# Optimization experiments

Hardware: AMD Instinct MI355X
Metric: run time of the kernel (lower is better)

Reference implementation:

```python
import jax, jax.numpy as jnp
import numpy as np

N_VOXELS = 1024
N_RAYS = 2048
SH_DEGREE = 2
N_SH = 9            # (sh_degree+1)^2 with degree-2 real SH basis (1+3+5 terms)
S = 8               # ray_samples_per_voxel
BG_COLOR = (0.0, 0.0, 0.0)
FAR_PLANE = 100.0
EARLY_STOP_T = 0.01 # transmittance early-termination threshold from the torch loop


def eval_sh_basis(degree, dirs):
    # dirs: [..., 3] -> [..., N_SH]
    x, y, z = dirs[..., 0], dirs[..., 1], dirs[..., 2]
    sh = [jnp.ones_like(x)]
    if degree >= 1:
        sh += [y, z, x]
    if degree >= 2:
        sh += [x * y, y * z, 3 * z ** 2 - 1, x * z, x ** 2 - y ** 2]
    if degree >= 3:
        sh += [y * (3 * x ** 2 - y ** 2), x * y * z, y * (5 * z ** 2 - 1),
               z * (5 * z ** 2 - 3), x * (5 * z ** 2 - 1), (x ** 2 - y ** 2) * z,
               x * (x ** 2 - 3 * y ** 2)]
    return jnp.stack(sh, axis=-1)


def setup_inputs() -> dict:
    key = jax.random.key(0)
    ks = jax.random.split(key, 6)
    positions = jax.random.uniform(ks[0], (N_VOXELS, 3), minval=-1.0, maxval=1.0)
    sizes = 0.05 + 0.15 * jax.random.uniform(ks[1], (N_VOXELS,))
    densities = jax.random.normal(ks[2], (N_VOXELS,))
    colors = 0.3 * jax.random.normal(ks[3], (N_VOXELS, 3 * N_SH))
    ray_origins = jnp.array([0.0, 0.0, -3.0]) + 0.1 * jax.random.normal(ks[4], (N_RAYS, 3))
    targets = jax.random.uniform(ks[5], (N_RAYS, 3), minval=-1.0, maxval=1.0)
    d = targets - ray_origins
    ray_directions = d / jnp.linalg.norm(d, axis=-1, keepdims=True)
    return {"positions": positions, "sizes": sizes, "densities": densities,
            "colors": colors, "ray_origins": ray_origins, "ray_directions": ray_directions}


def _forward(positions, sizes, densities, colors, ray_o, ray_d):
    B = ray_o.shape[0]
    N = positions.shape[0]
    # ---- AABB intersection for all (ray, voxel) pairs ----
    half = (sizes / 2.0)[:, None]                      # [N,1]
    bmin = positions - half                            # [N,3]
    bmax = positions + half
    inv_d = 1.0 / ray_d                                # [B,3]
    t0 = (bmin[None, :, :] - ray_o[:, None, :]) * inv_d[:, None, :]   # [B,N,3]
    t1 = (bmax[None, :, :] - ray_o[:, None, :]) * inv_d[:, None, :]
    t_near = jnp.max(jnp.minimum(t0, t1), axis=-1)     # [B,N]
    t_far = jnp.min(jnp.maximum(t0, t1), axis=-1)
    valid = (t_far > t_near) & (t_far > 0.0)
    # sanitize invalid entries so no inf/nan leaks into masked-out math
    tn = jnp.where(valid, t_near, 0.0)
    tf = jnp.where(valid, t_far, 1.0)

    # ---- per-ray SH color (rgb_samples is constant across samples: dirs = ray_d) ----
    sh = eval_sh_basis(SH_DEGREE, ray_d)               # [B,C]
    coeffs = colors.reshape(N, 3, N_SH)                # [N,3,C]
    rgb_vox = jax.nn.sigmoid(jnp.einsum('bc,nkc->bnk', sh, coeffs))   # [B,N,3]

    # ---- within-voxel alpha compositing (S samples, constant sigma per voxel) ----
    sigma = jnp.exp(densities)                         # [N], density_activation='exp'
    delta = (tf - tn) / S                              # [B,N]
    alpha = 1.0 - jnp.exp(-sigma[None, :] * delta)     # [B,N]
    base = 1.0 - alpha + 1e-8
    i = jnp.arange(S, dtype=jnp.float32)
    pw = base[..., None] ** i                          # [B,N,S] exclusive cumprod of (1-a)
    w = alpha[..., None] * pw                          # per-sample weights
    frac = i / (S - 1)                                 # linspace(t_near, t_far, S)
    t_s = tn[..., None] + (tf - tn)[..., None] * frac  # [B,N,S]
    ws = jnp.where(valid, jnp.sum(w, -1), 0.0)         # [B,N] weight_sum per voxel
    depth_vox = jnp.where(valid, jnp.sum(w * t_s, -1), 0.0)

    # ---- sort voxels per ray by entry distance (invalid -> end) ----
    key_t = jnp.where(valid, tn, jnp.inf)
    order = jnp.argsort(key_t, axis=-1)                # [B,N]
    ws_s = jnp.take_along_axis(ws, order, -1)
    dep_s = jnp.take_along_axis(depth_vox, order, -1)
    rgb_s = jnp.take_along_axis(rgb_vox, order[..., None], 1)

    # ---- sequential compositing across voxels (closed form, with early-stop mask) ----
    one_m = 1.0 - ws_s
    T_before = jnp.cumprod(
        jnp.concatenate([jnp.ones((B, 1), one_m.dtype), one_m[:, :-1]], -1), axis=-1)
    proc = (T_before >= EARLY_STOP_T).astype(one_m.dtype)  # voxels processed before break
    contrib = T_before * ws_s * proc                   # [B,N]
    rgb_acc = jnp.einsum('bn,bnk->bk', contrib, rgb_s) # [B,3]
    depth_acc = jnp.sum(T_before * proc * dep_s, -1)   # [B]
    weight_acc = jnp.sum(contrib, -1)                  # [B]
    T_final = jnp.prod(1.0 - ws_s * proc, -1)          # transmittance at break/end

    bg = jnp.asarray(BG_COLOR, dtype=rgb_acc.dtype)
    rgb_acc = rgb_acc + T_final[:, None] * bg
    has_hit = valid.any(-1)
    depth = jnp.where(has_hit, depth_acc, FAR_PLANE)[:, None]
    return rgb_acc, depth, weight_acc[:, None]


def reference(positions, sizes, densities, colors, ray_origins, ray_directions):
    return _forward(positions, sizes, densities, colors, ray_origins, ray_directions)
```

## Files before the change

### kernel.cpp

```cpp
#include <hip/hip_runtime.h>


#define BLOCK 256
#define CAP   128
#define EARLY_STOP 0.01f

__global__ __launch_bounds__(BLOCK) void voxel_raster(
    const float* __restrict__ positions, const float* __restrict__ sizes,
    const float* __restrict__ densities, const float* __restrict__ colors,
    const float* __restrict__ ray_o, const float* __restrict__ ray_d,
    float* __restrict__ out, int B)
{
    const int b   = blockIdx.x;
    const int tid = threadIdx.x;

    __shared__ int cnt;
    __shared__ unsigned long long key[CAP];
    __shared__ float h_ws[CAP], h_dep[CAP], h_r[CAP], h_g[CAP], h_b[CAP];

    if (tid == 0) cnt = 0;
    __syncthreads();

    const float ox = ray_o[b*3+0], oy = ray_o[b*3+1], oz = ray_o[b*3+2];
    const float dx = ray_d[b*3+0], dy = ray_d[b*3+1], dz = ray_d[b*3+2];
    const float ivx = 1.0f/dx, ivy = 1.0f/dy, ivz = 1.0f/dz;

    float sh[9];
    sh[0]=1.0f; sh[1]=dy; sh[2]=dz; sh[3]=dx;
    sh[4]=dx*dy; sh[5]=dy*dz; sh[6]=3.0f*dz*dz-1.0f; sh[7]=dx*dz; sh[8]=dx*dx-dy*dy;

    const float4 P0 = ((const float4*)positions)[tid*3+0];
    const float4 P1 = ((const float4*)positions)[tid*3+1];
    const float4 P2 = ((const float4*)positions)[tid*3+2];
    const float4 SZ = ((const float4*)sizes)[tid];

    const float pxa[4] = {P0.x, P0.w, P1.z, P2.y};
    const float pya[4] = {P0.y, P1.x, P1.w, P2.z};
    const float pza[4] = {P0.z, P1.y, P2.x, P2.w};
    const float hsa[4] = {SZ.x*0.5f, SZ.y*0.5f, SZ.z*0.5f, SZ.w*0.5f};

    #pragma unroll
    for (int k = 0; k < 4; ++k) {
        const int n = tid*4 + k;
        const float half = hsa[k];
        const float px = pxa[k], py = pya[k], pz = pza[k];

        float a0 = (px - half - ox) * ivx, a1 = (px + half - ox) * ivx;
        float tn = fminf(a0, a1), tf = fmaxf(a0, a1);
        a0 = (py - half - oy) * ivy; a1 = (py + half - oy) * ivy;
        tn = fmaxf(tn, fminf(a0, a1)); tf = fminf(tf, fmaxf(a0, a1));
        a0 = (pz - half - oz) * ivz; a1 = (pz + half - oz) * ivz;
        tn = fmaxf(tn, fminf(a0, a1)); tf = fminf(tf, fmaxf(a0, a1));

        if ((tf > tn) && (tf > 0.0f)) {
            const float sigma = __expf(densities[n]);
            const float dt    = tf - tn;
            const float alpha = 1.0f - __expf(-sigma * dt * 0.125f);
            const float base  = 1.0f - alpha + 1e-8f;
            float pw = 1.0f, ws = 0.0f, dep = 0.0f;
            #pragma unroll
            for (int i = 0; i < 8; i++) {
                const float w  = alpha * pw;
                const float ts = tn + dt * ((float)i * (1.0f / 7.0f));
                ws  += w;
                dep += w * ts;
                pw  *= base;
            }
            float rgb[3];
            #pragma unroll
            for (int c3 = 0; c3 < 3; c3++) {
                float acc = 0.0f;
                #pragma unroll
                for (int c = 0; c < 9; c++)
                    acc += sh[c] * colors[n*27 + c3*9 + c];
                rgb[c3] = __fdividef(1.0f, 1.0f + __expf(-acc));
            }

            const int slot = atomicAdd(&cnt, 1);
            if (slot < CAP) {
                unsigned u = __float_as_uint(tn);
                u = (u & 0x80000000u) ? ~u : (u | 0x80000000u);
                key[slot]   = ((unsigned long long)u << 32) | (unsigned)n;
                h_ws[slot]  = ws;
                h_dep[slot] = dep;
                h_r[slot]   = rgb[0];
                h_g[slot]   = rgb[1];
                h_b[slot]   = rgb[2];
            }
        }
    }
    __syncthreads();

    const int total = cnt;
    const int m = (total < CAP) ? total : CAP;

    if (tid < 64) {
        float ra = 0.f, ga = 0.f, ba = 0.f, da = 0.f, wa = 0.f;
        for (int l = tid; l < m; l += 64) {
            const unsigned long long kl = key[l];
            float Tb = 1.0f;
            for (int j = 0; j < m; ++j) {
                const unsigned long long kj = key[j];
                const float wj = h_ws[j];
                Tb *= (kj < kl) ? (1.0f - wj) : 1.0f;
            }
            if (Tb >= EARLY_STOP) {
                const float ws = h_ws[l];
                const float c  = Tb * ws;
                ra += c * h_r[l];
                ga += c * h_g[l];
                ba += c * h_b[l];
                da += Tb * h_dep[l];
                wa += c;
            }
        }
        #pragma unroll
        for (int off = 32; off > 0; off >>= 1) {
            ra += __shfl_down(ra, off, 64);
            ga += __shfl_down(ga, off, 64);
            ba += __shfl_down(ba, off, 64);
            da += __shfl_down(da, off, 64);
            wa += __shfl_down(wa, off, 64);
        }
        if (tid == 0) {
            out[b*3+0] = ra;
            out[b*3+1] = ga;
            out[b*3+2] = ba;
            out[B*3+b] = (total > 0) ? da : 100.0f;
            out[B*4+b] = wa;
        }
    }
}

extern "C" void kernel_launch(void* const* d_in, const int* in_sizes, int n_in,
                              void* d_out, int out_size, void* d_ws, size_t ws_size,
                              hipStream_t stream) {
    const float* positions = (const float*)d_in[0];
    const float* sizes     = (const float*)d_in[1];
    const float* densities = (const float*)d_in[2];
    const float* colors    = (const float*)d_in[3];
    const float* ray_o     = (const float*)d_in[4];
    const float* ray_d     = (const float*)d_in[5];
    const int B = in_sizes[4] / 3;

    voxel_raster<<<B, BLOCK, 0, stream>>>(
        positions, sizes, densities, colors, ray_o, ray_d, (float*)d_out, B);
}
```

Before: 69.94 us.

## Process four rays per block with one wavefront compositing each ray

Each block now handles four rays. Every thread intersects its four voxels against all four rays, and only the hit lists (tn, tf, key) go into shared memory. Afterwards each wavefront takes one ray and computes density weights and SH colors for that ray's hits, so the color work runs only on hits that pass early stop. Compositing is spread over all four wavefronts instead of leaving three idle, and voxel loads are amortized across rays. In exchange, per-thread register use rises (27 color values, ray arrays) and there are fewer blocks.

```diff
diff --git a/kernel.cpp b/kernel.cpp
--- a/kernel.cpp
+++ b/kernel.cpp
@@ -2,6 +2,7 @@
 
 
 #define BLOCK 256
+#define RPB   4
 #define CAP   128
 #define EARLY_STOP 0.01f
 
@@ -11,23 +12,17 @@
     const float* __restrict__ ray_o, const float* __restrict__ ray_d,
     float* __restrict__ out, int B)
 {
-    const int b   = blockIdx.x;
-    const int tid = threadIdx.x;
-
-    __shared__ int cnt;
-    __shared__ unsigned long long key[CAP];
-    __shared__ float h_ws[CAP], h_dep[CAP], h_r[CAP], h_g[CAP], h_b[CAP];
-
-    if (tid == 0) cnt = 0;
+    const int tid   = threadIdx.x;
+    const int lane  = tid & 63;
+    const int wv    = tid >> 6;
+    const int rbase = blockIdx.x * RPB;
+
+    __shared__ int cnt[RPB];
+    __shared__ unsigned long long key[RPB][CAP];
+    __shared__ float h_tn[RPB][CAP], h_tf[RPB][CAP], h_ws[RPB][CAP];
+
+    if (tid < RPB) cnt[tid] = 0;
     __syncthreads();
-
-    const float ox = ray_o[b*3+0], oy = ray_o[b*3+1], oz = ray_o[b*3+2];
-    const float dx = ray_d[b*3+0], dy = ray_d[b*3+1], dz = ray_d[b*3+2];
-    const float ivx = 1.0f/dx, ivy = 1.0f/dy, ivz = 1.0f/dz;
-
-    float sh[9];
-    sh[0]=1.0f; sh[1]=dy; sh[2]=dz; sh[3]=dx;
-    sh[4]=dx*dy; sh[5]=dy*dz; sh[6]=3.0f*dz*dz-1.0f; sh[7]=dx*dz; sh[8]=dx*dx-dy*dy;
 
     const float4 P0 = ((const float4*)positions)[tid*3+0];
     const float4 P1 = ((const float4*)positions)[tid*3+1];
@@ -39,81 +34,148 @@
     const float pza[4] = {P0.z, P1.y, P2.x, P2.w};
     const float hsa[4] = {SZ.x*0.5f, SZ.y*0.5f, SZ.z*0.5f, SZ.w*0.5f};
 
+    float rox[RPB], roy[RPB], roz[RPB], rix[RPB], riy[RPB], riz[RPB];
+    #pragma unroll
+    for (int r = 0; r < RPB; ++r) {
+        const int b = (rbase + r < B) ? (rbase + r) : 0;
+        rox[r] = ray_o[b*3+0]; roy[r] = ray_o[b*3+1]; roz[r] = ray_o[b*3+2];
+        rix[r] = 1.0f / ray_d[b*3+0];
+        riy[r] = 1.0f / ray_d[b*3+1];
+        riz[r] = 1.0f / ray_d[b*3+2];
+    }
+
     #pragma unroll
     for (int k = 0; k < 4; ++k) {
         const int n = tid*4 + k;
-        const float half = hsa[k];
-        const float px = pxa[k], py = pya[k], pz = pza[k];
-
-        float a0 = (px - half - ox) * ivx, a1 = (px + half - ox) * ivx;
-        float tn = fminf(a0, a1), tf = fmaxf(a0, a1);
-        a0 = (py - half - oy) * ivy; a1 = (py + half - oy) * ivy;
-        tn = fmaxf(tn, fminf(a0, a1)); tf = fminf(tf, fmaxf(a0, a1));
-        a0 = (pz - half - oz) * ivz; a1 = (pz + half - oz) * ivz;
-        tn = fmaxf(tn, fminf(a0, a1)); tf = fminf(tf, fmaxf(a0, a1));
-
-        if ((tf > tn) && (tf > 0.0f)) {
+        const float lox = pxa[k]-hsa[k], hix = pxa[k]+hsa[k];
+        const float loy = pya[k]-hsa[k], hiy = pya[k]+hsa[k];
+        const float loz = pza[k]-hsa[k], hiz = pza[k]+hsa[k];
+        #pragma unroll
+        for (int r = 0; r < RPB; ++r) {
+            float a0 = (lox - rox[r]) * rix[r], a1 = (hix - rox[r]) * rix[r];
+            float tn = fminf(a0, a1), tf = fmaxf(a0, a1);
+            a0 = (loy - roy[r]) * riy[r]; a1 = (hiy - roy[r]) * riy[r];
+            tn = fmaxf(tn, fminf(a0, a1)); tf = fminf(tf, fmaxf(a0, a1));
+            a0 = (loz - roz[r]) * riz[r]; a1 = (hiz - roz[r]) * riz[r];
+            tn = fmaxf(tn, fminf(a0, a1)); tf = fminf(tf, fmaxf(a0, a1));
+            if ((tf > tn) && (tf > 0.0f)) {
+                const int slot = atomicAdd(&cnt[r], 1);
+                if (slot < CAP) {
+                    unsigned u = __float_as_uint(tn);
+                    u = (u & 0x80000000u) ? ~u : (u | 0x80000000u);
+                    key[r][slot]  = ((unsigned long long)u << 32) | (unsigned)n;
+                    h_tn[r][slot] = tn;
+                    h_tf[r][slot] = tf;
+                }
+            }
+        }
+    }
+    __syncthreads();
+
+    const int b = rbase + wv;
+    if (b < B) {
+        const float dx = ray_d[b*3+0], dy = ray_d[b*3+1], dz = ray_d[b*3+2];
+        float sh[9];
+        sh[0]=1.0f; sh[1]=dy; sh[2]=dz; sh[3]=dx;
+        sh[4]=dx*dy; sh[5]=dy*dz; sh[6]=3.0f*dz*dz-1.0f; sh[7]=dx*dz; sh[8]=dx*dx-dy*dy;
+
+        const int total = cnt[wv];
+        const int m = (total < CAP) ? total : CAP;
+
+        float ws0 = 0.f, dep0 = 0.f, col0[27];
+        if (lane < m) {
+            const int n    = (int)(unsigned)key[wv][lane];
+            const float tn = h_tn[wv][lane], tf = h_tf[wv][lane];
             const float sigma = __expf(densities[n]);
             const float dt    = tf - tn;
             const float alpha = 1.0f - __expf(-sigma * dt * 0.125f);
             const float base  = 1.0f - alpha + 1e-8f;
-            float pw = 1.0f, ws = 0.0f, dep = 0.0f;
+            float pw = 1.0f, ws = 0.f, dep = 0.f;
             #pragma unroll
-            for (int i = 0; i < 8; i++) {
-                const float w  = alpha * pw;
-                const float ts = tn + dt * ((float)i * (1.0f / 7.0f));
+            for (int i = 0; i < 8; ++i) {
+                const float w = alpha * pw;
                 ws  += w;
-                dep += w * ts;
+                dep += w * (tn + dt * ((float)i * (1.0f / 7.0f)));
                 pw  *= base;
             }
-            float rgb[3];
+            h_ws[wv][lane] = ws;
+            ws0 = ws; dep0 = dep;
             #pragma unroll
-            for (int c3 = 0; c3 < 3; c3++) {
-                float acc = 0.0f;
-                #pragma unroll
-                for (int c = 0; c < 9; c++)
-                    acc += sh[c] * colors[n*27 + c3*9 + c];
-                rgb[c3] = __fdividef(1.0f, 1.0f + __expf(-acc));
-            }
-
-            const int slot = atomicAdd(&cnt, 1);
-            if (slot < CAP) {
-                unsigned u = __float_as_uint(tn);
-                u = (u & 0x80000000u) ? ~u : (u | 0x80000000u);
-                key[slot]   = ((unsigned long long)u << 32) | (unsigned)n;
-                h_ws[slot]  = ws;
-                h_dep[slot] = dep;
-                h_r[slot]   = rgb[0];
-                h_g[slot]   = rgb[1];
-                h_b[slot]   = rgb[2];
-            }
-        }
-    }
-    __syncthreads();
-
-    const int total = cnt;
-    const int m = (total < CAP) ? total : CAP;
-
-    if (tid < 64) {
+            for (int c = 0; c < 27; ++c)
+                col0[c] = colors[n*27 + c];
+        }
+        int nn1 = 0; float ws1 = 0.f, dep1 = 0.f;
+        if (lane + 64 < m) {
+            const int l    = lane + 64;
+            const int n    = (int)(unsigned)key[wv][l];
+            const float tn = h_tn[wv][l], tf = h_tf[wv][l];
+            const float sigma = __expf(densities[n]);
+            const float dt    = tf - tn;
+            const float alpha = 1.0f - __expf(-sigma * dt * 0.125f);
+            const float base  = 1.0f - alpha + 1e-8f;
+            float pw = 1.0f, ws = 0.f, dep = 0.f;
+            #pragma unroll
+            for (int i = 0; i < 8; ++i) {
+                const float w = alpha * pw;
+                ws  += w;
+                dep += w * (tn + dt * ((float)i * (1.0f / 7.0f)));
+                pw  *= base;
+            }
+            h_ws[wv][l] = ws;
+            nn1 = n; ws1 = ws; dep1 = dep;
+        }
+
         float ra = 0.f, ga = 0.f, ba = 0.f, da = 0.f, wa = 0.f;
-        for (int l = tid; l < m; l += 64) {
-            const unsigned long long kl = key[l];
+        if (lane < m) {
+            const unsigned long long kl = key[wv][lane];
             float Tb = 1.0f;
             for (int j = 0; j < m; ++j) {
-                const unsigned long long kj = key[j];
-                const float wj = h_ws[j];
+                const unsigned long long kj = key[wv][j];
+                const float wj = h_ws[wv][j];
                 Tb *= (kj < kl) ? (1.0f - wj) : 1.0f;
             }
             if (Tb >= EARLY_STOP) {
-                const float ws = h_ws[l];
-                const float c  = Tb * ws;
-                ra += c * h_r[l];
-                ga += c * h_g[l];
-                ba += c * h_b[l];
-                da += Tb * h_dep[l];
+                const float c = Tb * ws0;
+                float ar = 0.f, ag = 0.f, ab = 0.f;
+                #pragma unroll
+                for (int cc = 0; cc < 9; ++cc) {
+                    ar += sh[cc] * col0[cc];
+                    ag += sh[cc] * col0[9 + cc];
+                    ab += sh[cc] * col0[18 + cc];
+                }
+                ra += c * __fdividef(1.0f, 1.0f + __expf(-ar));
+                ga += c * __fdividef(1.0f, 1.0f + __expf(-ag));
+                ba += c * __fdividef(1.0f, 1.0f + __expf(-ab));
+                da += Tb * dep0;
                 wa += c;
             }
         }
+        if (lane + 64 < m) {
+            const int l = lane + 64;
+            const unsigned long long kl = key[wv][l];
+            float Tb = 1.0f;
+            for (int j = 0; j < m; ++j) {
+                const unsigned long long kj = key[wv][j];
+                const float wj = h_ws[wv][j];
+                Tb *= (kj < kl) ? (1.0f - wj) : 1.0f;
+            }
+            if (Tb >= EARLY_STOP) {
+                const float c = Tb * ws1;
+                float ar = 0.f, ag = 0.f, ab = 0.f;
+                #pragma unroll
+                for (int cc = 0; cc < 9; ++cc) {
+                    ar += sh[cc] * colors[nn1*27 + cc];
+                    ag += sh[cc] * colors[nn1*27 + 9 + cc];
+                    ab += sh[cc] * colors[nn1*27 + 18 + cc];
+                }
+                ra += c * __fdividef(1.0f, 1.0f + __expf(-ar));
+                ga += c * __fdividef(1.0f, 1.0f + __expf(-ag));
+                ba += c * __fdividef(1.0f, 1.0f + __expf(-ab));
+                da += Tb * dep1;
+                wa += c;
+            }
+        }
+
         #pragma unroll
         for (int off = 32; off > 0; off >>= 1) {
             ra += __shfl_down(ra, off, 64);
@@ -122,7 +184,7 @@
             da += __shfl_down(da, off, 64);
             wa += __shfl_down(wa, off, 64);
         }
-        if (tid == 0) {
+        if (lane == 0) {
             out[b*3+0] = ra;
             out[b*3+1] = ga;
             out[b*3+2] = ba;
@@ -143,6 +205,6 @@
     const float* ray_d     = (const float*)d_in[5];
     const int B = in_sizes[4] / 3;
 
-    voxel_raster<<<B, BLOCK, 0, stream>>>(
+    voxel_raster<<<(B + RPB - 1) / RPB, BLOCK, 0, stream>>>(
         positions, sizes, densities, colors, ray_o, ray_d, (float*)d_out, B);
 }
```

Result: faster. 68.27 us (-2.4%).
